# Kernel tuning notes

Measured on AMD Instinct MI355X. Metric: run time of the kernel, lower is better.

Reference implementation:

```python
import math
import jax, jax.numpy as jnp
import numpy as np

N_HEAD = 16
HEAD_DIM = 128


def _rope(x, cos, sin):
    # x: (B,T,H,D); cos,sin: (T,1,D/2) broadcast over B,H
    d = x.shape[-1] // 2
    x1, x2 = x[..., :d], x[..., d:]
    return jnp.concatenate([x1 * cos + x2 * sin, -x1 * sin + x2 * cos], axis=-1)


def _rms_norm(x, eps=1e-6):
    return x * jax.lax.rsqrt(jnp.mean(x * x, axis=-1, keepdims=True) + eps)


def setup_inputs() -> dict:
    key = jax.random.key(0)
    ks = jax.random.split(key, 9)
    B, T, C = 2, 2048, 2048
    scale = 1.0 / math.sqrt(C)
    return {
        "x": jax.random.normal(ks[0], (B, T, C), jnp.float32),
        "ve": jax.random.normal(ks[1], (B, T, C), jnp.float32),
        "Wq": jax.random.normal(ks[2], (C, C), jnp.float32) * scale,
        "Wk": jax.random.normal(ks[3], (C, C), jnp.float32) * scale,
        "Wv": jax.random.normal(ks[4], (C, C), jnp.float32) * scale,
        "Wproj": jax.random.normal(ks[5], (C, C), jnp.float32) * scale,
        "Wgate": jax.random.normal(ks[6], (N_HEAD, 12), jnp.float32) * (1.0 / math.sqrt(12.0)),
        "cos": jax.random.uniform(ks[7], (T, 1, HEAD_DIM // 2), jnp.float32),
        "sin": jax.random.uniform(ks[8], (T, 1, HEAD_DIM // 2), jnp.float32),
        "window_left": 1024,
    }


def reference(x, ve, Wq, Wk, Wv, Wproj, Wgate, cos, sin, window_left):
    B, T, C = x.shape
    H, D = N_HEAD, HEAD_DIM

    # Linear projections (torch Linear: x @ W.T)
    q = (x @ Wq.T).reshape(B, T, H, D)
    k = (x @ Wk.T).reshape(B, T, H, D)
    v = (x @ Wv.T).reshape(B, T, H, D)

    # value-embedding gating (has_ve layer)
    gate = 3.0 * jax.nn.sigmoid(x[..., :12] @ Wgate.T)  # (B,T,H)
    v = v + gate[..., None] * ve.reshape(B, T, H, D)

    # rope + qk rms-norm * 1.2
    q = _rms_norm(_rope(q, cos, sin)) * 1.2
    k = _rms_norm(_rope(k, cos, sin)) * 1.2

    # windowed causal mask
    row = jnp.arange(T)[:, None]
    col = jnp.arange(T)[None, :]
    mask = row >= col
    if 0 < window_left < T:
        mask = mask & (row - col <= window_left)
    bias = jnp.where(mask, 0.0, -1e9).astype(x.dtype)  # (T,T)

    scale = 1.0 / math.sqrt(D)
    att = jnp.einsum("bqhd,bkhd->bhqk", q, k) * scale + bias[None, None]
    att = jax.nn.softmax(att, axis=-1)
    y = jnp.einsum("bhqk,bkhd->bqhd", att, v).reshape(B, T, H * D)
    return y @ Wproj.T
```

## Files before the change

kernel.cpp:

```cpp
#include <hip/hip_runtime.h>
#include <hip/hip_bf16.h>
#include <cstdint>

#define N_HEAD 16
#define HEAD_DIM 128

typedef __bf16 bf16;
typedef __bf16 bf16x8 __attribute__((ext_vector_type(8)));
typedef __bf16 bf16x4 __attribute__((ext_vector_type(4)));
typedef float f32x4 __attribute__((ext_vector_type(4)));

__device__ __forceinline__ void gload_lds16(const void* g, void* l) {
  auto gp = reinterpret_cast<const __attribute__((address_space(1))) char*>(
      reinterpret_cast<uintptr_t>(g));
  auto lp = reinterpret_cast<__attribute__((address_space(3))) char*>(
      reinterpret_cast<uintptr_t>(l));
  __builtin_amdgcn_global_load_lds(gp, lp, 16, 0, 0);
}

__global__ __launch_bounds__(256) void cvt_all(
    const float* __restrict__ x, const float* __restrict__ Wq,
    const float* __restrict__ Wk, const float* __restrict__ Wv,
    const float* __restrict__ Wp, bf16* __restrict__ xb,
    bf16* __restrict__ wqkv, bf16* __restrict__ wpb, int nx4, int nw4) {
  const int z = blockIdx.z;
  const float* in;
  bf16* out;
  int n4;
  if (z == 0)      { in = x;  out = xb;  n4 = nx4; }
  else if (z == 1) { in = Wq; out = wqkv;                     n4 = nw4; }
  else if (z == 2) { in = Wk; out = wqkv + (size_t)nw4 * 4;   n4 = nw4; }
  else if (z == 3) { in = Wv; out = wqkv + (size_t)nw4 * 8;   n4 = nw4; }
  else             { in = Wp; out = wpb;  n4 = nw4; }
  const int i = blockIdx.x * 256 + threadIdx.x;
  if (i >= n4) return;
  const float4 f = reinterpret_cast<const float4*>(in)[i];
  bf16x4 o;
  o.x = (bf16)f.x; o.y = (bf16)f.y; o.z = (bf16)f.z; o.w = (bf16)f.w;
  reinterpret_cast<bf16x4*>(out)[i] = o;
}

template <typename OutT>
__global__ __launch_bounds__(256) void gemm_bt(
    const bf16* __restrict__ A, const bf16* __restrict__ Bt,
    OutT* __restrict__ C, int M, int N, int K) {
  __shared__ __align__(16) bf16 As[2][128 * 32];
  __shared__ __align__(16) bf16 Bs[2][128 * 32];
  const int tid = threadIdx.x;
  const int lane = tid & 63;
  const int wave = tid >> 6;
  const int wm = (wave >> 1) * 64;
  const int wn = (wave & 1) * 64;
  const int lr = lane & 15;
  const int lk = (lane >> 4) * 8;

  const bf16* Ab = A + (size_t)blockIdx.y * 128 * K;
  const bf16* Bb = Bt + (size_t)blockIdx.x * 128 * K;

  const int r0 = tid >> 2;
  const int c0 = (tid & 3) * 8;

  f32x4 acc[4][4] = {};

  for (int k0 = 0; k0 < K; k0 += 64) {
    __syncthreads();
#pragma unroll
    for (int s = 0; s < 2; ++s) {
      const int kk = k0 + s * 32 + c0;
      gload_lds16(Ab + (size_t)r0 * K + kk, As[s] + (size_t)tid * 8);
      gload_lds16(Ab + (size_t)(r0 + 64) * K + kk, As[s] + (size_t)(256 + tid) * 8);
      gload_lds16(Bb + (size_t)r0 * K + kk, Bs[s] + (size_t)tid * 8);
      gload_lds16(Bb + (size_t)(r0 + 64) * K + kk, Bs[s] + (size_t)(256 + tid) * 8);
    }
    __syncthreads();

#pragma unroll
    for (int s = 0; s < 2; ++s) {
      bf16x8 a[4], b[4];
#pragma unroll
      for (int i = 0; i < 4; ++i)
        a[i] = *reinterpret_cast<const bf16x8*>(As[s] + (wm + i * 16 + lr) * 32 + lk);
#pragma unroll
      for (int j = 0; j < 4; ++j)
        b[j] = *reinterpret_cast<const bf16x8*>(Bs[s] + (wn + j * 16 + lr) * 32 + lk);
#pragma unroll
      for (int i = 0; i < 4; ++i)
#pragma unroll
        for (int j = 0; j < 4; ++j)
          acc[i][j] = __builtin_amdgcn_mfma_f32_16x16x32_bf16(a[i], b[j], acc[i][j], 0, 0, 0);
    }
  }

  const int orow = blockIdx.y * 128 + wm + (lane >> 4) * 4;
  const int ocol = blockIdx.x * 128 + wn + lr;
#pragma unroll
  for (int i = 0; i < 4; ++i)
#pragma unroll
    for (int j = 0; j < 4; ++j)
#pragma unroll
      for (int r = 0; r < 4; ++r)
        C[(size_t)(orow + i * 16 + r) * N + (ocol + j * 16)] = (OutT)acc[i][j][r];
}

__global__ __launch_bounds__(256) void rope_rms(
    bf16* __restrict__ qkv, const float* __restrict__ cs,
    const float* __restrict__ sn, int T) {
  const int C = N_HEAD * HEAD_DIM;
  const int S = 3 * C;
  const int bt = blockIdx.x;
  const int t = bt % T;
  const int wave = threadIdx.x >> 6;
  const int lane = threadIdx.x & 63;
  const int h = blockIdx.y * 4 + wave;
  bf16* p = qkv + (size_t)bt * S + (blockIdx.z ? C : 0) + h * HEAD_DIM;
  const float oscale = blockIdx.z ? 1.2f : 0.15302091809294977f;
  const float c = cs[t * 64 + lane];
  const float s = sn[t * 64 + lane];
  const float x1 = (float)p[lane];
  const float x2 = (float)p[lane + 64];
  const float r1 = x1 * c + x2 * s;
  const float r2 = x2 * c - x1 * s;
  float ss = r1 * r1 + r2 * r2;
#pragma unroll
  for (int m = 1; m < 64; m <<= 1) ss += __shfl_xor(ss, m);
  const float sc = oscale * rsqrtf(ss * (1.0f / 128.0f) + 1e-6f);
  p[lane] = (bf16)(r1 * sc);
  p[lane + 64] = (bf16)(r2 * sc);
}

__global__ __launch_bounds__(256) void gate_transpose(
    const bf16* __restrict__ qkv, const float* __restrict__ x,
    const float* __restrict__ ve, const float* __restrict__ Wg,
    bf16* __restrict__ vT, int T) {
  const int C = N_HEAD * HEAD_DIM;
  const int S = 3 * C;
  const int t0 = blockIdx.x * 64;
  const int c0 = blockIdx.y * 64;
  const int b = blockIdx.z;
  const int h = c0 >> 7;

  __shared__ float gs[64];
  __shared__ __align__(16) bf16 tile[64][72];

  if (threadIdx.x < 64) {
    const float* xr = x + (size_t)(b * T + t0 + threadIdx.x) * C;
    float a = 0.f;
#pragma unroll
    for (int j = 0; j < 12; ++j) a += xr[j] * Wg[h * 12 + j];
    gs[threadIdx.x] = 3.f / (1.f + __expf(-a));
  }
  __syncthreads();

  {
    const int r = threadIdx.x >> 2;
    const int cc = (threadIdx.x & 3) * 16;
    const size_t vrow = (size_t)(b * T + t0 + r) * S + 2 * C + c0 + cc;
    const size_t erow = (size_t)(b * T + t0 + r) * C + c0 + cc;
    bf16x8 a0 = *reinterpret_cast<const bf16x8*>(qkv + vrow);
    bf16x8 a1 = *reinterpret_cast<const bf16x8*>(qkv + vrow + 8);
    const float g = gs[r];
    bf16x8 o0, o1;
#pragma unroll
    for (int i = 0; i < 8; ++i) o0[i] = (bf16)((float)a0[i] + g * ve[erow + i]);
#pragma unroll
    for (int i = 0; i < 8; ++i) o1[i] = (bf16)((float)a1[i] + g * ve[erow + 8 + i]);
    *reinterpret_cast<bf16x8*>(&tile[r][cc]) = o0;
    *reinterpret_cast<bf16x8*>(&tile[r][cc + 8]) = o1;
  }
  __syncthreads();
  {
    const int dr = threadIdx.x >> 2;
    const int tc = (threadIdx.x & 3) * 16;
    bf16x8 o0, o1;
#pragma unroll
    for (int i = 0; i < 8; ++i) o0[i] = tile[tc + i][dr];
#pragma unroll
    for (int i = 0; i < 8; ++i) o1[i] = tile[tc + 8 + i][dr];
    const size_t orow =
        ((size_t)((b * N_HEAD + h) * HEAD_DIM) + (c0 & 127) + dr) * T + t0 + tc;
    *reinterpret_cast<bf16x8*>(vT + orow) = o0;
    *reinterpret_cast<bf16x8*>(vT + orow + 8) = o1;
  }
}

__global__ __launch_bounds__(256, 2) void attn(
    const bf16* __restrict__ qkv, const bf16* __restrict__ vT,
    bf16* __restrict__ y, const int* __restrict__ wptr, int T, int B) {
  const int C = N_HEAD * HEAD_DIM;
  const int S = 3 * C;
  const int nq = T >> 7;
  const int ppx = (B * N_HEAD) >> 3;
  const int bid = blockIdx.x;
  const int xcd = bid & 7;
  const int sl = bid >> 3;
  const int pair = xcd * ppx + sl / nq;
  const int qi = sl % nq;
  const int b = pair / N_HEAD;
  const int h = pair % N_HEAD;
  const int qb = qi * 128;

  const int tid = threadIdx.x;
  const int wave = tid >> 6;
  const int lane = tid & 63;
  const int lm = lane & 15;
  const int quad = lane >> 4;

  const int w = wptr[0];
  const int W = (w > 0 && w < T) ? w : (1 << 30);

  __shared__ __align__(16) bf16 Ks[4][64][32];
  __shared__ __align__(16) bf16 Vs[2][128][32];
  __shared__ __align__(16) bf16 Pb[4][16][72];

  const bf16* kb = qkv + (size_t)b * T * S + C + (size_t)h * HEAD_DIM;
  const bf16* vb = vT + (size_t)((b * N_HEAD + h) * HEAD_DIM) * T;

  const int qt[2] = {qb + wave * 16, qb + 64 + wave * 16};
  bf16x8 qf[2][4];
#pragma unroll
  for (int t = 0; t < 2; ++t) {
    const bf16* qrow = qkv + (size_t)(b * T + qt[t] + lm) * S + h * HEAD_DIM;
#pragma unroll
    for (int c = 0; c < 4; ++c)
      qf[t][c] = *reinterpret_cast<const bf16x8*>(qrow + c * 32 + quad * 8);
  }

  float mrun[2] = {-1e30f, -1e30f}, lrun[2] = {0.f, 0.f};
  f32x4 oacc[2][8] = {};

  int kstart = qb - W;
  if (kstart < 0) kstart = 0;
  kstart &= ~63;
  const int kend = qb + 64;

  const int sr = tid >> 2;
  const int sc = (tid & 3) * 8;

  bf16x8 kpre[4], vpre[4];
  {
    const bf16* kr = kb + (size_t)(kstart + sr) * S + sc;
#pragma unroll
    for (int c = 0; c < 4; ++c)
      kpre[c] = *reinterpret_cast<const bf16x8*>(kr + c * 32);
#pragma unroll
    for (int c2 = 0; c2 < 2; ++c2)
#pragma unroll
      for (int i = 0; i < 2; ++i)
        vpre[c2 * 2 + i] = *reinterpret_cast<const bf16x8*>(
            vb + (size_t)(i * 64 + sr) * T + kstart + c2 * 32 + sc);
  }

  for (int kc = kstart; kc <= kend; kc += 64) {
    __syncthreads();
#pragma unroll
    for (int c = 0; c < 4; ++c)
      *reinterpret_cast<bf16x8*>(&Ks[c][sr][sc]) = kpre[c];
#pragma unroll
    for (int c2 = 0; c2 < 2; ++c2)
#pragma unroll
      for (int i = 0; i < 2; ++i)
        *reinterpret_cast<bf16x8*>(&Vs[c2][i * 64 + sr][sc]) = vpre[c2 * 2 + i];
    __syncthreads();

    if (kc + 64 <= kend) {
      const int kc2 = kc + 64;
      const bf16* kr = kb + (size_t)(kc2 + sr) * S + sc;
#pragma unroll
      for (int c = 0; c < 4; ++c)
        kpre[c] = *reinterpret_cast<const bf16x8*>(kr + c * 32);
#pragma unroll
      for (int c2 = 0; c2 < 2; ++c2)
#pragma unroll
        for (int i = 0; i < 2; ++i)
          vpre[c2 * 2 + i] = *reinterpret_cast<const bf16x8*>(
              vb + (size_t)(i * 64 + sr) * T + kc2 + c2 * 32 + sc);
    }

#pragma unroll
    for (int t = 0; t < 2; ++t) {
      const int q0 = qt[t];
      if (kc > q0 + 15 || kc + 63 < q0 - W) continue;
      const int qr = q0 + lm;

      f32x4 st[4] = {};
#pragma unroll
      for (int g = 0; g < 4; ++g)
#pragma unroll
        for (int c = 0; c < 4; ++c) {
          const bf16x8 kf =
              *reinterpret_cast<const bf16x8*>(&Ks[c][g * 16 + lm][quad * 8]);
          st[g] = __builtin_amdgcn_mfma_f32_16x16x32_bf16(kf, qf[t][c], st[g], 0, 0, 0);
        }
      float mx = -1e30f;
#pragma unroll
      for (int g = 0; g < 4; ++g)
#pragma unroll
        for (int r = 0; r < 4; ++r) {
          const int key = kc + g * 16 + quad * 4 + r;
          const bool valid = (key <= qr) && (qr - key <= W);
          st[g][r] = valid ? st[g][r] : -1e30f;
          mx = fmaxf(mx, st[g][r]);
        }
      mx = fmaxf(mx, __shfl_xor(mx, 16));
      mx = fmaxf(mx, __shfl_xor(mx, 32));
      const float mnew = fmaxf(mrun[t], mx);
      const float alpha = __builtin_amdgcn_exp2f(mrun[t] - mnew);
      mrun[t] = mnew;
      float rs = 0.f;
#pragma unroll
      for (int g = 0; g < 4; ++g) {
        bf16x4 pk;
#pragma unroll
        for (int r = 0; r < 4; ++r) {
          const float p = __builtin_amdgcn_exp2f(st[g][r] - mnew);
          rs += p;
          pk[r] = (bf16)p;
        }
        *reinterpret_cast<bf16x4*>(&Pb[wave][lm][g * 16 + quad * 4]) = pk;
      }
      rs += __shfl_xor(rs, 16);
      rs += __shfl_xor(rs, 32);
      lrun[t] = lrun[t] * alpha + rs;
#pragma unroll
      for (int dc = 0; dc < 8; ++dc)
#pragma unroll
        for (int r = 0; r < 4; ++r) oacc[t][dc][r] *= alpha;
#pragma unroll
      for (int c2 = 0; c2 < 2; ++c2) {
        const bf16x8 pf =
            *reinterpret_cast<const bf16x8*>(&Pb[wave][lm][c2 * 32 + quad * 8]);
#pragma unroll
        for (int dc = 0; dc < 8; ++dc) {
          const bf16x8 vf =
              *reinterpret_cast<const bf16x8*>(&Vs[c2][dc * 16 + lm][quad * 8]);
          oacc[t][dc] = __builtin_amdgcn_mfma_f32_16x16x32_bf16(vf, pf, oacc[t][dc], 0, 0, 0);
        }
      }
    }
  }

#pragma unroll
  for (int t = 0; t < 2; ++t) {
    const float inv = 1.f / lrun[t];
    bf16* yr = y + (size_t)(b * T + qt[t] + lm) * C + h * HEAD_DIM;
#pragma unroll
    for (int dc = 0; dc < 8; ++dc) {
      bf16x4 o;
#pragma unroll
      for (int r = 0; r < 4; ++r) o[r] = (bf16)(oacc[t][dc][r] * inv);
      *reinterpret_cast<bf16x4*>(yr + dc * 16 + quad * 4) = o;
    }
  }
}

extern "C" void kernel_launch(void* const* d_in, const int* in_sizes, int n_in,
                              void* d_out, int out_size, void* d_ws, size_t ws_size,
                              hipStream_t stream) {
  const float* x  = (const float*)d_in[0];
  const float* ve = (const float*)d_in[1];
  const float* Wq = (const float*)d_in[2];
  const float* Wk = (const float*)d_in[3];
  const float* Wv = (const float*)d_in[4];
  const float* Wp = (const float*)d_in[5];
  const float* Wg = (const float*)d_in[6];
  const float* cs = (const float*)d_in[7];
  const float* sn = (const float*)d_in[8];
  const int*   wl = (const int*)d_in[9];
  float* out = (float*)d_out;

  const int C = N_HEAD * HEAD_DIM;
  const int T = in_sizes[7] / (HEAD_DIM / 2);
  const int B = in_sizes[0] / (T * C);
  const int M = B * T;

  bf16* xb   = (bf16*)d_ws;
  bf16* wqkv = xb   + (size_t)M * C;
  bf16* wpb  = wqkv + (size_t)3 * C * C;
  bf16* qkv  = wpb  + (size_t)C * C;
  bf16* ybuf = qkv  + (size_t)3 * M * C;
  bf16* vTb  = xb;

  const int nx4 = M * C / 4, nw4 = C * C / 4;
  cvt_all<<<dim3((nx4 + 255) / 256, 1, 5), 256, 0, stream>>>(
      x, Wq, Wk, Wv, Wp, xb, wqkv, wpb, nx4, nw4);

  gemm_bt<bf16><<<dim3(3 * C / 128, M / 128), 256, 0, stream>>>(xb, wqkv, qkv, M, 3 * C, C);

  rope_rms<<<dim3(M, N_HEAD / 4, 2), 256, 0, stream>>>(qkv, cs, sn, T);
  gate_transpose<<<dim3(T / 64, C / 64, B), 256, 0, stream>>>(qkv, x, ve, Wg, vTb, T);
  attn<<<dim3(B * N_HEAD * (T / 128)), 256, 0, stream>>>(qkv, vTb, ybuf, wl, T, B);

  gemm_bt<float><<<dim3(C / 128, M / 128), 256, 0, stream>>>(ybuf, wpb, out, M, C, C);
}
```

Before: 435.6 us.

## Replace QKV projection GEMM with 256x256-tile pipelined double-buffered kernel

```diff
diff --git a/kernel.cpp b/kernel.cpp
--- a/kernel.cpp
+++ b/kernel.cpp
@@ -102,6 +102,131 @@
         C[(size_t)(orow + i * 16 + r) * N + (ocol + j * 16)] = (OutT)acc[i][j][r];
 }
 
+__global__ __launch_bounds__(512, 2) void gemm256(
+    const bf16* __restrict__ A, const bf16* __restrict__ Bt,
+    bf16* __restrict__ C, int M, int N, int K) {
+  __shared__ __align__(16) char sA[2][32768];
+  __shared__ __align__(16) char sB[2][32768];
+
+  const int nwgy = M >> 8;
+  const int nwg = (N >> 8) * nwgy;
+  const int q8 = nwg >> 3;
+  const int wgid = (blockIdx.x & 7) * q8 + (blockIdx.x >> 3);
+  const int by = wgid % nwgy;
+  const int bx = wgid / nwgy;
+
+  const int tid = threadIdx.x;
+  const int lane = tid & 63;
+  const int wave = tid >> 6;
+  const int wm = (wave >> 2) << 7;
+  const int wn = (wave & 3) << 6;
+  const int lr = lane & 15;
+  const int lk16 = (lane >> 4) << 4;
+  const int sx = (lr & 7) << 4;
+
+  const bf16* Ab = A + (size_t)by * 256 * K;
+  const bf16* Bb = Bt + (size_t)bx * 256 * K;
+
+  int srow[2], scol[2];
+#pragma unroll
+  for (int pp = 0; pp < 2; ++pp) {
+    const int o = pp * 8192 + tid * 16;
+    srow[pp] = o >> 7;
+    scol[pp] = (o & 127) ^ ((srow[pp] & 7) << 4);
+  }
+
+  auto stageA = [&](int buf, int half, int k0) {
+#pragma unroll
+    for (int pp = 0; pp < 2; ++pp)
+      gload_lds16(Ab + (size_t)(half * 128 + srow[pp]) * K + k0 + (scol[pp] >> 1),
+                  sA[buf] + half * 16384 + pp * 8192 + tid * 16);
+  };
+  auto stageB = [&](int buf, int half, int k0) {
+#pragma unroll
+    for (int pp = 0; pp < 2; ++pp)
+      gload_lds16(Bb + (size_t)(half * 128 + srow[pp]) * K + k0 + (scol[pp] >> 1),
+                  sB[buf] + half * 16384 + pp * 8192 + tid * 16);
+  };
+
+  f32x4 acc[8][4] = {};
+  bf16x8 bF[4][2];
+
+#define VMCNT4                                             \
+  asm volatile("s_waitcnt vmcnt(4)" ::: "memory");         \
+  __builtin_amdgcn_sched_barrier(0)
+#define VMCNT0                                             \
+  asm volatile("s_waitcnt vmcnt(0)" ::: "memory");         \
+  __builtin_amdgcn_sched_barrier(0)
+
+#define PHASE(BUF, P, STAGE, WAIT)                                             \
+  {                                                                            \
+    bf16x8 aF[2][2];                                                           \
+    if (P == 0) {                                                              \
+      _Pragma("unroll") for (int n = 0; n < 4; ++n)                            \
+      _Pragma("unroll") for (int ks = 0; ks < 2; ++ks)                         \
+        bF[n][ks] = *reinterpret_cast<const bf16x8*>(                          \
+            sB[BUF] + (wn + n * 16 + lr) * 128 + ((ks * 64 + lk16) ^ sx));     \
+    }                                                                          \
+    _Pragma("unroll") for (int mi = 0; mi < 2; ++mi)                           \
+    _Pragma("unroll") for (int ks = 0; ks < 2; ++ks)                           \
+      aF[mi][ks] = *reinterpret_cast<const bf16x8*>(                           \
+          sA[BUF] + (wm + (P * 2 + mi) * 16 + lr) * 128 +                      \
+          ((ks * 64 + lk16) ^ sx));                                            \
+    STAGE;                                                                     \
+    WAIT;                                                                      \
+    __builtin_amdgcn_s_barrier();                                              \
+    __builtin_amdgcn_s_setprio(1);                                             \
+    _Pragma("unroll") for (int ks = 0; ks < 2; ++ks)                           \
+    _Pragma("unroll") for (int mi = 0; mi < 2; ++mi)                           \
+    _Pragma("unroll") for (int n = 0; n < 4; ++n)                              \
+      acc[P * 2 + mi][n] = __builtin_amdgcn_mfma_f32_16x16x32_bf16(            \
+          aF[mi][ks], bF[n][ks], acc[P * 2 + mi][n], 0, 0, 0);                 \
+    __builtin_amdgcn_s_setprio(0);                                             \
+    __builtin_amdgcn_s_barrier();                                              \
+  }
+
+  const int nIt = K >> 7;
+
+  stageB(0, 0, 0); stageB(0, 1, 0);
+  stageA(0, 0, 0); stageA(0, 1, 0);
+  stageB(1, 0, 64); stageB(1, 1, 64);
+  VMCNT4;
+  __builtin_amdgcn_s_barrier();
+
+  int k0 = 0;
+  for (int it = 0; it < nIt - 1; ++it, k0 += 128) {
+    PHASE(0, 0, stageA(1, 0, k0 + 64), );
+    PHASE(0, 1, stageA(1, 1, k0 + 64), );
+    PHASE(0, 2, stageB(0, 0, k0 + 128), );
+    PHASE(0, 3, stageB(0, 1, k0 + 128), VMCNT4);
+    PHASE(1, 0, stageA(0, 0, k0 + 128), );
+    PHASE(1, 1, stageA(0, 1, k0 + 128), );
+    PHASE(1, 2, stageB(1, 0, k0 + 192), );
+    PHASE(1, 3, stageB(1, 1, k0 + 192), VMCNT4);
+  }
+  PHASE(0, 0, stageA(1, 0, k0 + 64), );
+  PHASE(0, 1, stageA(1, 1, k0 + 64), );
+  PHASE(0, 2, , );
+  PHASE(0, 3, , VMCNT0);
+  PHASE(1, 0, , );
+  PHASE(1, 1, , );
+  PHASE(1, 2, , );
+  PHASE(1, 3, , );
+#undef PHASE
+#undef VMCNT4
+#undef VMCNT0
+
+  const int orow = by * 256 + wm + (lane >> 4) * 4;
+  const int ocol = bx * 256 + wn + lr;
+#pragma unroll
+  for (int m = 0; m < 8; ++m)
+#pragma unroll
+    for (int n = 0; n < 4; ++n)
+#pragma unroll
+      for (int r = 0; r < 4; ++r)
+        C[(size_t)(orow + m * 16 + r) * N + (ocol + n * 16)] = (bf16)acc[m][n][r];
+}
+
 __global__ __launch_bounds__(256) void rope_rms(
     bf16* __restrict__ qkv, const float* __restrict__ cs,
     const float* __restrict__ sn, int T) {
@@ -384,7 +509,8 @@
   cvt_all<<<dim3((nx4 + 255) / 256, 1, 5), 256, 0, stream>>>(
       x, Wq, Wk, Wv, Wp, xb, wqkv, wpb, nx4, nw4);
 
-  gemm_bt<bf16><<<dim3(3 * C / 128, M / 128), 256, 0, stream>>>(xb, wqkv, qkv, M, 3 * C, C);
+  gemm256<<<dim3((3 * C / 256) * (M / 256)), 512, 0, stream>>>(
+      xb, wqkv, qkv, M, 3 * C, C);
 
   rope_rms<<<dim3(M, N_HEAD / 4, 2), 256, 0, stream>>>(qkv, cs, sn, T);
   gate_transpose<<<dim3(T / 64, C / 64, B), 256, 0, stream>>>(qkv, x, ve, Wg, vTb, T);
```

New measurement: 418.6 us. 1.04x faster.
